# Kernel tuning notes

Measured on AMD Instinct MI355X. Metric: run time of the kernel, lower is better.

## Reference

```python
import jax, jax.numpy as jnp
import numpy as np

S = 3072       # packed sequence length
DIM = 1280     # hidden dim
H = 16         # num heads
HD = DIM // H  # head dim = 80
NEG = -1e9     # additive mask value for cross-segment entries


def setup_inputs() -> dict:
    key = jax.random.key(0)
    ks = jax.random.split(key, 6)
    x = jax.random.normal(ks[0], (S, DIM), jnp.float32)
    # rope angle table [S, HD//2]
    rotary_pos_emb = jax.random.uniform(ks[1], (S, HD // 2), jnp.float32, 0.0, 2.0 * np.pi)
    # 4 equal image segments packed together
    cu_seqlens = jnp.array([0, 768, 1536, 2304, 3072], jnp.int32)
    w_qkv = jax.random.normal(ks[2], (3 * DIM, DIM), jnp.float32) * 0.02
    b_qkv = jax.random.normal(ks[3], (3 * DIM,), jnp.float32) * 0.02
    w_proj = jax.random.normal(ks[4], (DIM, DIM), jnp.float32) * 0.02
    b_proj = jax.random.normal(ks[5], (DIM,), jnp.float32) * 0.02
    return {"x": x, "cu_seqlens": cu_seqlens, "rotary_pos_emb": rotary_pos_emb,
            "w_qkv": w_qkv, "b_qkv": b_qkv, "w_proj": w_proj, "b_proj": b_proj}


def _rope(t, cos, sin):
    # t: [S, H, HD]; cos/sin: [S, 1, HD]
    t1, t2 = jnp.split(t, 2, axis=-1)
    rot = jnp.concatenate([-t2, t1], axis=-1)
    return t * cos + rot * sin


def reference(x, cu_seqlens, rotary_pos_emb, w_qkv, b_qkv, w_proj, b_proj):
    s, d = x.shape
    qkv = (x @ w_qkv.T + b_qkv).reshape(s, 3, H, HD)
    q, k, v = qkv[:, 0], qkv[:, 1], qkv[:, 2]  # each [S, H, HD]

    # NeoX-style rope with tiled (repeated) freqs, computed in fp32
    cos = jnp.cos(rotary_pos_emb)
    sin = jnp.sin(rotary_pos_emb)
    cos = jnp.concatenate([cos, cos], axis=-1)[:, None, :]  # [S,1,HD]
    sin = jnp.concatenate([sin, sin], axis=-1)[:, None, :]
    q = _rope(q.astype(jnp.float32), cos, sin).astype(x.dtype)
    k = _rope(k.astype(jnp.float32), cos, sin).astype(x.dtype)

    # block-diagonal varlen mask from cu_seqlens: segment id per position
    seg = jnp.searchsorted(cu_seqlens, jnp.arange(s), side='right') - 1  # [S]
    mask = jnp.where(seg[:, None] == seg[None, :], 0.0, NEG).astype(x.dtype)  # [S,S]

    scale = 1.0 / np.sqrt(HD).astype(np.float32)
    scores = jnp.einsum('qhd,khd->hqk', q, k) * scale + mask[None]  # [H,S,S]
    attn = jax.nn.softmax(scores, axis=-1)
    out = jnp.einsum('hqk,khd->qhd', attn, v).reshape(s, d)  # [S, DIM]
    return out @ w_proj.T + b_proj
```

## Files before the change

kernel.cpp:

```cpp
#include <hip/hip_runtime.h>


typedef __bf16 bf16;
typedef __bf16 bf16x4 __attribute__((ext_vector_type(4)));
typedef __bf16 bf16x8 __attribute__((ext_vector_type(8)));
typedef float f32x4 __attribute__((ext_vector_type(4)));
typedef float f32x16 __attribute__((ext_vector_type(16)));
typedef unsigned int u32;

constexpr int S = 3072;
constexpr int DIM = 1280;
constexpr int H = 16;
constexpr int HD = 80;
constexpr int KDP = 128;
constexpr int NQKV = 3 * DIM;

constexpr int MB_A = S / 256;
constexpr int NB_B = NQKV / 256;
constexpr int NKT = DIM / 32;

constexpr float QSCALE = 1.4426950408889634f / 8.94427190999916f;

__device__ __forceinline__ void gload_lds16(const void* g, void* l) {
  __builtin_amdgcn_global_load_lds(
      (const __attribute__((address_space(1))) void*)g,
      (__attribute__((address_space(3))) void*)l, 16, 0, 0);
}

__device__ __forceinline__ u32 pkbf2(float a, float b) {
  union { bf16 h[2]; u32 w; } u;
  u.h[0] = (bf16)a; u.h[1] = (bf16)b;
  return u.w;
}

__device__ __forceinline__ int swv(int s) {
  return ((((s >> 3) & 31) ^ ((s & 7) << 2)) << 2);
}

constexpr long PA_CHUNKS = (long)MB_A * NKT * 1024;
constexpr long PB_CHUNKS = (long)NB_B * NKT * 1024;
constexpr long PW_CHUNKS = (long)DIM * DIM / 8;
constexpr long KP_CHUNKS = (long)H * S * 48 / 8;
constexpr long CS_CHUNKS = (long)S * 40 / 8;
constexpr long TOT_CHUNKS = PA_CHUNKS + PB_CHUNKS + PW_CHUNKS + KP_CHUNKS + CS_CHUNKS;

__global__ __launch_bounds__(256) void pack_inputs(
    const float* __restrict__ x, const float* __restrict__ wq,
    const float* __restrict__ wp, const float* __restrict__ rope,
    bf16* __restrict__ pA, bf16* __restrict__ pB, bf16* __restrict__ wp16,
    bf16* __restrict__ Kb, float* __restrict__ ctab, float* __restrict__ stab) {
  long t = (long)blockIdx.x * 256 + threadIdx.x;
  if (t < PA_CHUNKS + PB_CHUNKS) {
    int blk, rem;
    const float* base;
    bf16* obase;
    bool isB = false;
    if (t < PA_CHUNKS) {
      blk = (int)(t / (NKT * 1024)); rem = (int)(t % (NKT * 1024));
      base = x; obase = pA + t * 8;
    } else {
      long t2 = t - PA_CHUNKS;
      blk = (int)(t2 / (NKT * 1024)); rem = (int)(t2 % (NKT * 1024));
      base = wq; obase = pB + t2 * 8;
      isB = true;
    }
    const int kt = rem >> 10, c = rem & 1023;
    const int lin = c * 16;
    const int logi = lin ^ (((lin >> 7) & 7) << 4);
    int row = logi >> 6;
    const int col = (logi & 63) >> 1;
    int grow = blk * 256 + row;
    if (isB && grow < 2560) {
      const int ty = grow / 1280, rm = grow % 1280;
      const int h = rm / 80, p = rm % 80;
      grow = ty * 1280 + h * 80 + (p >> 1) + (p & 1) * 40;
    }
    const float* src = base + (size_t)grow * DIM + kt * 32 + col;
    float4 v0 = *(const float4*)src;
    float4 v1 = *(const float4*)(src + 4);
    bf16x8 o = {(bf16)v0.x, (bf16)v0.y, (bf16)v0.z, (bf16)v0.w,
                (bf16)v1.x, (bf16)v1.y, (bf16)v1.z, (bf16)v1.w};
    *(bf16x8*)obase = o;
  } else if (t < PA_CHUNKS + PB_CHUNKS + PW_CHUNKS) {
    long t2 = t - PA_CHUNKS - PB_CHUNKS;
    const float* src = wp + t2 * 8;
    float4 v0 = *(const float4*)src;
    float4 v1 = *(const float4*)(src + 4);
    bf16x8 o = {(bf16)v0.x, (bf16)v0.y, (bf16)v0.z, (bf16)v0.w,
                (bf16)v1.x, (bf16)v1.y, (bf16)v1.z, (bf16)v1.w};
    *(bf16x8*)(wp16 + t2 * 8) = o;
  } else if (t < PA_CHUNKS + PB_CHUNKS + PW_CHUNKS + KP_CHUNKS) {
    long t2 = t - PA_CHUNKS - PB_CHUNKS - PW_CHUNKS;
    const int h = (int)(t2 / (S * 6)), r = (int)(t2 % (S * 6));
    const int s = r / 6, cc = r % 6;
    bf16x8 z = {};
    *(bf16x8*)(Kb + ((size_t)h * S + s) * KDP + 80 + cc * 8) = z;
  } else {
    long t3 = t - PA_CHUNKS - PB_CHUNKS - PW_CHUNKS - KP_CHUNKS;
#pragma unroll
    for (int k = 0; k < 8; k++) {
      const int idx = (int)(t3 * 8 + k);
      const int s = idx / 40, a = idx % 40;
      float sn, cs;
      __sincosf(rope[idx], &sn, &cs);
      ctab[a * S + s] = cs;
      stab[a * S + s] = sn;
    }
  }
}

__global__ __launch_bounds__(512, 2) void gemm256(
    const bf16* __restrict__ pA, const bf16* __restrict__ pB,
    const float* __restrict__ bias, const float* __restrict__ ctab,
    const float* __restrict__ stab, bf16* __restrict__ Qb,
    bf16* __restrict__ Kb, bf16* __restrict__ VTb) {
  extern __shared__ char lds[];
  const int tid = threadIdx.x;
  const int w = tid >> 6, lane = tid & 63;
  const int r15 = lane & 15, b4 = lane >> 4;
  const int wr = w >> 2, wc = w & 3;
  const int nwg = gridDim.x * gridDim.y;
  const int orig = blockIdx.y * gridDim.x + blockIdx.x;
  const int xcd = orig % 8, loc = orig / 8;
  const int qq = nwg / 8, rq = nwg % 8;
  const int swzid =
      (xcd < rq ? xcd * (qq + 1) : rq * (qq + 1) + (xcd - rq) * qq) + loc;
  const int nb = swzid % gridDim.x, mb = swzid / gridDim.x;
  const int m0 = mb * 256;
  const char* aPanel = (const char*)pA + (size_t)mb * NKT * 16384;
  const char* bPanel = (const char*)pB + (size_t)nb * NKT * 16384;
  auto stageA = [&](int kt) {
    char* s = lds + (kt & 3) * 32768;
    const char* g = aPanel + (size_t)kt * 16384;
    gload_lds16(g + tid * 16, s + tid * 16);
    gload_lds16(g + 8192 + tid * 16, s + 8192 + tid * 16);
  };
  auto stageB = [&](int kt) {
    char* s = lds + (kt & 3) * 32768 + 16384;
    const char* g = bPanel + (size_t)kt * 16384;
    gload_lds16(g + tid * 16, s + tid * 16);
    gload_lds16(g + 8192 + tid * 16, s + 8192 + tid * 16);
  };
  f32x4 acc[8][4] = {};
  stageA(0); stageB(0); stageA(1); stageB(1); stageA(2); stageB(2);
  asm volatile("s_waitcnt vmcnt(8)" ::: "memory");
  __builtin_amdgcn_s_barrier();
  for (int kt = 0; kt < NKT; ++kt) {
    const char* As = lds + (kt & 3) * 32768;
    const char* Bs = As + 16384;
    const bool pf = (kt + 3 < NKT);
    bf16x8 afr[4], bfr[4];
#pragma unroll
    for (int i = 0; i < 4; i++) {
      int a = (wr * 128 + i * 16 + r15) * 64 + b4 * 16;
      a ^= ((a >> 7) & 7) << 4;
      afr[i] = *(const bf16x8*)(As + a);
    }
#pragma unroll
    for (int j = 0; j < 4; j++) {
      int a = (wc * 64 + j * 16 + r15) * 64 + b4 * 16;
      a ^= ((a >> 7) & 7) << 4;
      bfr[j] = *(const bf16x8*)(Bs + a);
    }
    if (pf) stageA(kt + 3);
    asm volatile("" ::: "memory");
    __builtin_amdgcn_s_barrier();
    __builtin_amdgcn_s_setprio(1);
#pragma unroll
    for (int i = 0; i < 4; i++)
#pragma unroll
      for (int j = 0; j < 4; j++)
        acc[i][j] = __builtin_amdgcn_mfma_f32_16x16x32_bf16(afr[i], bfr[j],
                                                            acc[i][j], 0, 0, 0);
    __builtin_amdgcn_s_setprio(0);
    asm volatile("" ::: "memory");
    __builtin_amdgcn_s_barrier();
#pragma unroll
    for (int i = 0; i < 4; i++) {
      int a = (wr * 128 + 64 + i * 16 + r15) * 64 + b4 * 16;
      a ^= ((a >> 7) & 7) << 4;
      afr[i] = *(const bf16x8*)(As + a);
    }
    if (pf) stageB(kt + 3);
    asm volatile("" ::: "memory");
    __builtin_amdgcn_s_barrier();
    __builtin_amdgcn_s_setprio(1);
#pragma unroll
    for (int i = 0; i < 4; i++)
#pragma unroll
      for (int j = 0; j < 4; j++)
        acc[4 + i][j] = __builtin_amdgcn_mfma_f32_16x16x32_bf16(
            afr[i], bfr[j], acc[4 + i][j], 0, 0, 0);
    __builtin_amdgcn_s_setprio(0);
    const int rem = NKT - 2 - kt;
    if (rem >= 2)      asm volatile("s_waitcnt vmcnt(8)" ::: "memory");
    else if (rem == 1) asm volatile("s_waitcnt vmcnt(4)" ::: "memory");
    else if (rem == 0) asm volatile("s_waitcnt vmcnt(0)" ::: "memory");
    else               asm volatile("" ::: "memory");
    __builtin_amdgcn_s_barrier();
  }
  const int n0 = nb * 256;
  const int type = n0 / 1280;
  const int cpart0 = n0 - type * 1280;
  if (type < 2) {
#pragma unroll
    for (int j = 0; j < 4; j++) {
      const int c = wc * 64 + j * 16 + r15;
      const int cp = cpart0 + c;
      const int h = cp / 80, p = cp % 80;
      const int d = (p >> 1) + (p & 1) * 40;
      const float bv = bias[type * 1280 + h * 80 + d];
      const int a = p >> 1;
#pragma unroll
      for (int i = 0; i < 8; i++) {
        const int sl = wr * 128 + i * 16 + b4 * 4;
        f32x4 cs4 = *(const f32x4*)&ctab[a * S + m0 + sl];
        f32x4 sn4 = *(const f32x4*)&stab[a * S + m0 + sl];
#pragma unroll
        for (int r = 0; r < 4; r++) {
          float v = acc[i][j][r] + bv;
          float ov = __shfl_xor(v, 1);
          float res = (p & 1) ? (v * cs4[r] + ov * sn4[r])
                              : (v * cs4[r] - ov * sn4[r]);
          if (type == 0) res *= QSCALE;
          *(bf16*)(lds + (sl + r) * 512 + ((2 * c) ^ (((sl + r) & 7) << 4))) =
              (bf16)res;
        }
      }
    }
    __syncthreads();
#pragma unroll
    for (int t = 0; t < 16; t++) {
      const int task = t * 512 + tid;
      const int sl = task >> 5, c = (task & 31) * 8;
      bf16x8 v = *(const bf16x8*)(lds + sl * 512 + ((2 * c) ^ ((sl & 7) << 4)));
      const int cp = cpart0 + c, h = cp / 80, p = cp % 80;
      bf16* dst = type ? Kb + ((size_t)h * S + m0 + sl) * KDP + p
                       : Qb + ((size_t)h * S + m0 + sl) * HD + p;
      *(bf16x8*)dst = v;
    }
  } else {
#pragma unroll
    for (int j = 0; j < 4; j++) {
      const int c = wc * 64 + j * 16 + r15;
      const float bv = bias[2560 + cpart0 + c];
#pragma unroll
      for (int i = 0; i < 8; i++) {
        const int sl = wr * 128 + i * 16 + b4 * 4;
#pragma unroll
        for (int r = 0; r < 4; r++) {
          *(bf16*)(lds + (sl + r) * 512 + ((2 * c) ^ swv(sl + r))) =
              (bf16)(acc[i][j][r] + bv);
        }
      }
    }
    __syncthreads();
#pragma unroll
    for (int t = 0; t < 16; t++) {
      const int task = t * 512 + tid;
      const int c = task >> 5, s0 = (task & 31) * 8;
      union { bf16 h[8]; bf16x8 v; } o;
#pragma unroll
      for (int e = 0; e < 8; e++)
        o.h[e] = *(const bf16*)(lds + (s0 + e) * 512 + ((2 * c) ^ swv(s0 + e)));
      const int cp = cpart0 + c, h = cp / 80, d = cp % 80;
      *(bf16x8*)(VTb + ((size_t)(h * 80 + d)) * S + m0 + s0) = o.v;
    }
  }
}

__global__ __launch_bounds__(256) void gemm_proj(
    const bf16* __restrict__ A, const bf16* __restrict__ B,
    const float* __restrict__ bias, float* __restrict__ Cout, int M, int N,
    int K) {
  __shared__ bf16 Al[2][64 * 32];
  __shared__ bf16 Bl[2][128 * 32];
  const int tid = threadIdx.x;
  const int w = tid >> 6, lane = tid & 63;
  const int r15 = lane & 15, b4 = lane >> 4;
  const int nwg = gridDim.x * gridDim.y;
  const int orig = blockIdx.y * gridDim.x + blockIdx.x;
  const int swzid = (orig & 7) * (nwg >> 3) + (orig >> 3);
  const int bx = swzid % gridDim.x, by = swzid / gridDim.x;
  const int m0 = by * 64, n0 = bx * 128;
  const int wm = (w >> 1) * 32, wn = (w & 1) * 64;
  f32x4 acc[2][4] = {};
  const int row0 = tid >> 2, ko0 = (tid & 3) * 8;
  const bf16* Ar = A + (size_t)(m0 + row0) * K + ko0;
  const bf16* Br0 = B + (size_t)(n0 + row0) * K + ko0;
  const bf16* Br1 = B + (size_t)(n0 + row0 + 64) * K + ko0;

  auto stage = [&](int buf, int k0) {
    gload_lds16(Ar + k0, (char*)Al[buf] + tid * 16);
    gload_lds16(Br0 + k0, (char*)Bl[buf] + tid * 16);
    gload_lds16(Br1 + k0, (char*)Bl[buf] + 4096 + tid * 16);
  };

  stage(0, 0);
  int cur = 0;
  for (int k0 = 0; k0 < K; k0 += 32) {
    __syncthreads();
    if (k0 + 32 < K) stage(cur ^ 1, k0 + 32);
    bf16x8 af[2], bfr[4];
#pragma unroll
    for (int i = 0; i < 2; i++)
      af[i] = *(const bf16x8*)((const char*)Al[cur] + (wm + i * 16 + r15) * 64 + b4 * 16);
#pragma unroll
    for (int j = 0; j < 4; j++)
      bfr[j] = *(const bf16x8*)((const char*)Bl[cur] + (wn + j * 16 + r15) * 64 + b4 * 16);
#pragma unroll
    for (int i = 0; i < 2; i++)
#pragma unroll
      for (int j = 0; j < 4; j++)
        acc[i][j] = __builtin_amdgcn_mfma_f32_16x16x32_bf16(af[i], bfr[j], acc[i][j], 0, 0, 0);
    cur ^= 1;
  }
#pragma unroll
  for (int j = 0; j < 4; j++) {
    const int n = n0 + wn + j * 16 + r15;
    const float bv = bias[n];
#pragma unroll
    for (int i = 0; i < 2; i++) {
      const int mr = m0 + wm + i * 16 + b4 * 4;
#pragma unroll
      for (int r = 0; r < 4; r++)
        Cout[(size_t)(mr + r) * N + n] = acc[i][j][r] + bv;
    }
  }
}

__global__ __launch_bounds__(256) void attn_kern(
    const bf16* __restrict__ Qg, const bf16* __restrict__ Kg,
    const bf16* __restrict__ Vg, const int* __restrict__ cu, int nseg,
    bf16* __restrict__ Out) {
  __shared__ bf16 Kl[2][64 * 128];
  __shared__ bf16 Vl[2][96 * 64];
  const int tid = threadIdx.x, w = tid >> 6, lane = tid & 63;
  const int r31 = lane & 31, hi = lane >> 5;
  const int nwg = gridDim.x;
  const int orig = blockIdx.x;
  const int swzb = (orig & 7) * (nwg >> 3) + (orig >> 3);
  const int h = swzb / 24, qb = swzb % 24;
  const int q = qb * 128 + w * 32 + r31;
  int sq = 0, eq = S, lo = 0, hik = S;
  {
    const int qlo = qb * 128, qhi = qb * 128 + 127;
#pragma unroll
    for (int i = 0; i < 8; i++) {
      if (i >= nseg) break;
      int a = cu[i], b = cu[i + 1];
      if (q >= a && q < b) { sq = a; eq = b; }
      if (qlo >= a && qlo < b) lo = a;
      if (qhi >= a && qhi < b) hik = b;
    }
  }
  {
    int b = tid >> 7, o = (tid & 127) * 16;
    bf16x8 z = {};
    *(bf16x8*)((char*)Vl[b] + 10240 + o) = z;
  }
  bf16x8 qf[5];
  {
    const bf16* qrow = Qg + ((size_t)h * S + q) * HD + hi * 8;
#pragma unroll
    for (int kk = 0; kk < 5; kk++) qf[kk] = *(const bf16x8*)(qrow + kk * 16);
  }
  int kdst[4], ksrc[4], vdst[3], vsrc[3];
#pragma unroll
  for (int c = 0; c < 4; c++) {
    int lin = (c * 256 + tid) * 16;
    int row = lin >> 8, colb = (lin & 255) ^ ((row & 15) << 4);
    kdst[c] = lin; ksrc[c] = row * KDP + colb / 2;
  }
#pragma unroll
  for (int c = 0; c < 3; c++) {
    int lin = (c * 256 + tid) * 16;
    int row = lin >> 7, colb = (lin & 127) ^ ((row & 7) << 4);
    vdst[c] = lin; vsrc[c] = row * S + colb / 2;
  }
  const bf16* Kbase = Kg + (size_t)h * S * KDP;
  const bf16* Vbase = Vg + (size_t)h * HD * S;
  auto stage = [&](int buf, int k0) {
#pragma unroll
    for (int c = 0; c < 4; c++)
      gload_lds16(Kbase + (size_t)k0 * KDP + ksrc[c], (char*)Kl[buf] + kdst[c]);
#pragma unroll
    for (int c = 0; c < 3; c++)
      if (c < 2 || tid < 128)
        gload_lds16(Vbase + vsrc[c] + k0, (char*)Vl[buf] + vdst[c]);
  };
  f32x16 o0 = {}, o1 = {}, o2 = {};
  float m = -1e30f, l = 0.f;
  const int k0s = lo & ~63;
  stage(0, k0s);
  asm volatile("s_waitcnt vmcnt(0)" ::: "memory");
  __syncthreads();
  int cur = 0;
  for (int k0 = k0s; k0 < hik; k0 += 64) {
    const bool more = (k0 + 64 < hik);
    if (more) stage(cur ^ 1, k0 + 64);
    f32x16 st0 = {}, st1 = {};
    __builtin_amdgcn_s_setprio(1);
#pragma unroll
    for (int kk = 0; kk < 5; kk++) {
      const int colb = kk * 32 + hi * 16;
      bf16x8 kf0 = *(const bf16x8*)((const char*)Kl[cur] +
                                    r31 * 256 + (colb ^ ((r31 & 15) << 4)));
      bf16x8 kf1 = *(const bf16x8*)((const char*)Kl[cur] + (32 + r31) * 256 +
                                    (colb ^ ((r31 & 15) << 4)));
      st0 = __builtin_amdgcn_mfma_f32_32x32x16_bf16(kf0, qf[kk], st0, 0, 0, 0);
      st1 = __builtin_amdgcn_mfma_f32_32x32x16_bf16(kf1, qf[kk], st1, 0, 0, 0);
    }
    __builtin_amdgcn_s_setprio(0);
    float tm = -3e38f;
    if (k0 >= sq && k0 + 63 < eq) {
#pragma unroll
      for (int j = 0; j < 16; j++) {
        tm = fmaxf(tm, st0[j]);
        tm = fmaxf(tm, st1[j]);
      }
    } else {
#pragma unroll
      for (int j = 0; j < 16; j++) {
        const int crow = (j & 3) + 8 * (j >> 2) + 4 * hi;
        int key0 = k0 + crow, key1 = k0 + 32 + crow;
        st0[j] = (key0 >= sq && key0 < eq) ? st0[j] : -1e30f;
        st1[j] = (key1 >= sq && key1 < eq) ? st1[j] : -1e30f;
        tm = fmaxf(tm, st0[j]);
        tm = fmaxf(tm, st1[j]);
      }
    }
    tm = fmaxf(tm, __shfl_xor(tm, 32));
    if (!__all(tm <= m + 8.f)) {
      const float mn = fmaxf(m, tm);
      const float alpha = __builtin_amdgcn_exp2f(m - mn);
      o0 *= alpha; o1 *= alpha; o2 *= alpha;
      l *= alpha;
      m = mn;
    }
    float rs = 0.f;
    u32 wd0[4][2], wd1[4][2];
#pragma unroll
    for (int g2 = 0; g2 < 4; g2++) {
#pragma unroll
      for (int hh = 0; hh < 2; hh++) {
        float a0 = __builtin_amdgcn_exp2f(st0[g2 * 4 + 2 * hh] - m);
        float a1 = __builtin_amdgcn_exp2f(st0[g2 * 4 + 2 * hh + 1] - m);
        float b0 = __builtin_amdgcn_exp2f(st1[g2 * 4 + 2 * hh] - m);
        float b1 = __builtin_amdgcn_exp2f(st1[g2 * 4 + 2 * hh + 1] - m);
        rs += a0 + a1 + b0 + b1;
        wd0[g2][hh] = pkbf2(a0, a1);
        wd1[g2][hh] = pkbf2(b0, b1);
      }
    }
    rs += __shfl_xor(rs, 32);
    l += rs;
    __builtin_amdgcn_s_setprio(1);
#pragma unroll
    for (int kk = 0; kk < 4; kk++) {
      const int g2o = (kk & 1) * 2 + hi;
      const int g2s = (kk & 1) * 2 + (hi ^ 1);
      u32 own0, own1, snd0, snd1;
      if (kk < 2) {
        own0 = wd0[g2o][0]; own1 = wd0[g2o][1];
        snd0 = wd0[g2s][0]; snd1 = wd0[g2s][1];
      } else {
        own0 = wd1[g2o][0]; own1 = wd1[g2o][1];
        snd0 = wd1[g2s][0]; snd1 = wd1[g2s][1];
      }
      u32 rc0 = (u32)__shfl_xor((int)snd0, 32);
      u32 rc1 = (u32)__shfl_xor((int)snd1, 32);
      union { u32 w[4]; bf16x8 v; } pf;
      if (hi == 0) { pf.w[0] = own0; pf.w[1] = own1; pf.w[2] = rc0; pf.w[3] = rc1; }
      else         { pf.w[0] = rc0;  pf.w[1] = rc1;  pf.w[2] = own0; pf.w[3] = own1; }
      const int colb = kk * 32 + hi * 16;
#pragma unroll
      for (int mt = 0; mt < 3; mt++) {
        const int row = mt * 32 + r31;
        bf16x8 vf = *(const bf16x8*)((const char*)Vl[cur] + row * 128 +
                                     (colb ^ ((row & 7) << 4)));
        f32x16 * op = mt == 0 ? &o0 : (mt == 1 ? &o1 : &o2);
        *op = __builtin_amdgcn_mfma_f32_32x32x16_bf16(vf, pf.v, *op, 0, 0, 0);
      }
    }
    __builtin_amdgcn_s_setprio(0);
    asm volatile("s_waitcnt vmcnt(0)" ::: "memory");
    __syncthreads();
    cur ^= 1;
  }
  const float inv = 1.f / l;
  bf16* orow = Out + (size_t)q * DIM + h * HD;
#pragma unroll
  for (int rg = 0; rg < 4; rg++) {
    bf16x4 v0 = {(bf16)(o0[rg * 4] * inv), (bf16)(o0[rg * 4 + 1] * inv),
                 (bf16)(o0[rg * 4 + 2] * inv), (bf16)(o0[rg * 4 + 3] * inv)};
    *(bf16x4*)(orow + 8 * rg + 4 * hi) = v0;
    bf16x4 v1 = {(bf16)(o1[rg * 4] * inv), (bf16)(o1[rg * 4 + 1] * inv),
                 (bf16)(o1[rg * 4 + 2] * inv), (bf16)(o1[rg * 4 + 3] * inv)};
    *(bf16x4*)(orow + 32 + 8 * rg + 4 * hi) = v1;
  }
#pragma unroll
  for (int rg = 0; rg < 2; rg++) {
    bf16x4 v2 = {(bf16)(o2[rg * 4] * inv), (bf16)(o2[rg * 4 + 1] * inv),
                 (bf16)(o2[rg * 4 + 2] * inv), (bf16)(o2[rg * 4 + 3] * inv)};
    *(bf16x4*)(orow + 64 + 8 * rg + 4 * hi) = v2;
  }
}

extern "C" void kernel_launch(void* const* d_in, const int* in_sizes, int n_in,
                              void* d_out, int out_size, void* d_ws,
                              size_t ws_size, hipStream_t stream) {
  const float* x = (const float*)d_in[0];
  const int* cu = (const int*)d_in[1];
  const float* rope = (const float*)d_in[2];
  const float* w_qkv = (const float*)d_in[3];
  const float* b_qkv = (const float*)d_in[4];
  const float* w_proj = (const float*)d_in[5];
  const float* b_proj = (const float*)d_in[6];
  const int nseg = in_sizes[1] - 1;

  bf16* pA = (bf16*)d_ws;
  bf16* pB = pA + (size_t)S * DIM;
  bf16* wp16 = pB + (size_t)NQKV * DIM;
  bf16* Qb = wp16 + (size_t)DIM * DIM;
  bf16* Kb = Qb + (size_t)H * S * HD;
  bf16* VTb = Kb + (size_t)H * S * KDP;
  float* ctab = (float*)(VTb + (size_t)H * HD * S);
  float* stab = ctab + (size_t)S * 40;
  bf16* attn16 = pA;

  pack_inputs<<<(int)(TOT_CHUNKS / 256), 256, 0, stream>>>(
      x, w_qkv, w_proj, rope, pA, pB, wp16, Kb, ctab, stab);
  gemm256<<<dim3(NB_B, MB_A), 512, 131072, stream>>>(
      pA, pB, b_qkv, ctab, stab, Qb, Kb, VTb);
  attn_kern<<<H * 24, 256, 0, stream>>>(Qb, Kb, VTb, cu, nseg, attn16);
  gemm_proj<<<dim3(DIM / 128, S / 64), 256, 0, stream>>>(
      attn16, wp16, b_proj, (float*)d_out, S, DIM, DIM);
}
```

Baseline: 126.5 us.

## Load K/V fragments directly from global memory instead of LDS double buffering

The attention kernel drops its LDS staging buffers, the async global-to-LDS copies and the per-iteration barriers. Each wave now reads its K and V MFMA fragments straight from global memory, relying on the cache, with rows beyond the head dim clamped to row 0. Launch bounds are set to 3 blocks per SM to raise occupancy. The cost is redundant global and L2 traffic across the 4 waves sharing the same K/V tile, plus higher register pressure from holding 12 V fragments.

```diff
diff --git a/kernel.cpp b/kernel.cpp
--- a/kernel.cpp
+++ b/kernel.cpp
@@ -329,12 +329,10 @@
   }
 }
 
-__global__ __launch_bounds__(256) void attn_kern(
+__global__ __launch_bounds__(256, 3) void attn_kern(
     const bf16* __restrict__ Qg, const bf16* __restrict__ Kg,
     const bf16* __restrict__ Vg, const int* __restrict__ cu, int nseg,
     bf16* __restrict__ Out) {
-  __shared__ bf16 Kl[2][64 * 128];
-  __shared__ bf16 Vl[2][96 * 64];
   const int tid = threadIdx.x, w = tid >> 6, lane = tid & 63;
   const int r31 = lane & 31, hi = lane >> 5;
   const int nwg = gridDim.x;
@@ -354,64 +352,37 @@
       if (qhi >= a && qhi < b) hik = b;
     }
   }
-  {
-    int b = tid >> 7, o = (tid & 127) * 16;
-    bf16x8 z = {};
-    *(bf16x8*)((char*)Vl[b] + 10240 + o) = z;
-  }
   bf16x8 qf[5];
   {
     const bf16* qrow = Qg + ((size_t)h * S + q) * HD + hi * 8;
 #pragma unroll
     for (int kk = 0; kk < 5; kk++) qf[kk] = *(const bf16x8*)(qrow + kk * 16);
   }
-  int kdst[4], ksrc[4], vdst[3], vsrc[3];
-#pragma unroll
-  for (int c = 0; c < 4; c++) {
-    int lin = (c * 256 + tid) * 16;
-    int row = lin >> 8, colb = (lin & 255) ^ ((row & 15) << 4);
-    kdst[c] = lin; ksrc[c] = row * KDP + colb / 2;
-  }
-#pragma unroll
-  for (int c = 0; c < 3; c++) {
-    int lin = (c * 256 + tid) * 16;
-    int row = lin >> 7, colb = (lin & 127) ^ ((row & 7) << 4);
-    vdst[c] = lin; vsrc[c] = row * S + colb / 2;
-  }
   const bf16* Kbase = Kg + (size_t)h * S * KDP;
   const bf16* Vbase = Vg + (size_t)h * HD * S;
-  auto stage = [&](int buf, int k0) {
-#pragma unroll
-    for (int c = 0; c < 4; c++)
-      gload_lds16(Kbase + (size_t)k0 * KDP + ksrc[c], (char*)Kl[buf] + kdst[c]);
-#pragma unroll
-    for (int c = 0; c < 3; c++)
-      if (c < 2 || tid < 128)
-        gload_lds16(Vbase + vsrc[c] + k0, (char*)Vl[buf] + vdst[c]);
-  };
   f32x16 o0 = {}, o1 = {}, o2 = {};
   float m = -1e30f, l = 0.f;
-  const int k0s = lo & ~63;
-  stage(0, k0s);
-  asm volatile("s_waitcnt vmcnt(0)" ::: "memory");
-  __syncthreads();
-  int cur = 0;
-  for (int k0 = k0s; k0 < hik; k0 += 64) {
-    const bool more = (k0 + 64 < hik);
-    if (more) stage(cur ^ 1, k0 + 64);
+  for (int k0 = lo & ~63; k0 < hik; k0 += 64) {
     f32x16 st0 = {}, st1 = {};
-    __builtin_amdgcn_s_setprio(1);
 #pragma unroll
     for (int kk = 0; kk < 5; kk++) {
-      const int colb = kk * 32 + hi * 16;
-      bf16x8 kf0 = *(const bf16x8*)((const char*)Kl[cur] +
-                                    r31 * 256 + (colb ^ ((r31 & 15) << 4)));
-      bf16x8 kf1 = *(const bf16x8*)((const char*)Kl[cur] + (32 + r31) * 256 +
-                                    (colb ^ ((r31 & 15) << 4)));
+      const int ce = kk * 16 + hi * 8;
+      bf16x8 kf0 = *(const bf16x8*)(Kbase + (size_t)(k0 + r31) * KDP + ce);
+      bf16x8 kf1 = *(const bf16x8*)(Kbase + (size_t)(k0 + 32 + r31) * KDP + ce);
       st0 = __builtin_amdgcn_mfma_f32_32x32x16_bf16(kf0, qf[kk], st0, 0, 0, 0);
       st1 = __builtin_amdgcn_mfma_f32_32x32x16_bf16(kf1, qf[kk], st1, 0, 0, 0);
     }
-    __builtin_amdgcn_s_setprio(0);
+    bf16x8 vf[4][3];
+#pragma unroll
+    for (int kk = 0; kk < 4; kk++) {
+      const int ke = k0 + kk * 16 + hi * 8;
+#pragma unroll
+      for (int mt = 0; mt < 3; mt++) {
+        int row = mt * 32 + r31;
+        row = row < HD ? row : 0;
+        vf[kk][mt] = *(const bf16x8*)(Vbase + (size_t)row * S + ke);
+      }
+    }
     float tm = -3e38f;
     if (k0 >= sq && k0 + 63 < eq) {
 #pragma unroll
@@ -455,7 +426,6 @@
     }
     rs += __shfl_xor(rs, 32);
     l += rs;
-    __builtin_amdgcn_s_setprio(1);
 #pragma unroll
     for (int kk = 0; kk < 4; kk++) {
       const int g2o = (kk & 1) * 2 + hi;
@@ -473,20 +443,10 @@
       union { u32 w[4]; bf16x8 v; } pf;
       if (hi == 0) { pf.w[0] = own0; pf.w[1] = own1; pf.w[2] = rc0; pf.w[3] = rc1; }
       else         { pf.w[0] = rc0;  pf.w[1] = rc1;  pf.w[2] = own0; pf.w[3] = own1; }
-      const int colb = kk * 32 + hi * 16;
-#pragma unroll
-      for (int mt = 0; mt < 3; mt++) {
-        const int row = mt * 32 + r31;
-        bf16x8 vf = *(const bf16x8*)((const char*)Vl[cur] + row * 128 +
-                                     (colb ^ ((row & 7) << 4)));
-        f32x16 * op = mt == 0 ? &o0 : (mt == 1 ? &o1 : &o2);
-        *op = __builtin_amdgcn_mfma_f32_32x32x16_bf16(vf, pf.v, *op, 0, 0, 0);
-      }
-    }
-    __builtin_amdgcn_s_setprio(0);
-    asm volatile("s_waitcnt vmcnt(0)" ::: "memory");
-    __syncthreads();
-    cur ^= 1;
+      o0 = __builtin_amdgcn_mfma_f32_32x32x16_bf16(vf[kk][0], pf.v, o0, 0, 0, 0);
+      o1 = __builtin_amdgcn_mfma_f32_32x32x16_bf16(vf[kk][1], pf.v, o1, 0, 0, 0);
+      o2 = __builtin_amdgcn_mfma_f32_32x32x16_bf16(vf[kk][2], pf.v, o2, 0, 0, 0);
+    }
   }
   const float inv = 1.f / l;
   bf16* orow = Out + (size_t)q * DIM + h * HD;
```

New measurement: 162.4 us. 1.28x slower.
